# Performance work log

Measured on AMD Instinct MI355X. Metric: run time of the kernel, lower is better.

The kernel has to match this reference:

```python
import jax, jax.numpy as jnp
import numpy as np

B, H, W = 64, 224, 224
EPS = 1e-5


def setup_inputs() -> dict:
    key = jax.random.key(0)
    ks = jax.random.split(key, 8)
    n = lambda k, s, std: jax.random.normal(k, s, jnp.float32) * std
    return {
        "x": jax.random.normal(ks[0], (B, 1, H, W), jnp.float32),
        "conv1_w": n(ks[1], (24, 1, 3, 3), 0.2),
        "conv1_b": jnp.zeros((24,), jnp.float32),
        "bn1_g": jnp.ones((24,), jnp.float32),
        "bn1_b": jnp.zeros((24,), jnp.float32),
        "conv2_w": n(ks[2], (48, 24, 3, 3), 0.07),
        "conv2_b": jnp.zeros((48,), jnp.float32),
        "bn2_g": jnp.ones((48,), jnp.float32),
        "bn2_b": jnp.zeros((48,), jnp.float32),
        "fconv_w": n(ks[3], (48, 48, 56, 56), 0.003),
        "fconv_b": jnp.zeros((48,), jnp.float32),
        "lin1_w": n(ks[4], (24, 48), 0.02),
        "lin1_b": jnp.zeros((24,), jnp.float32),
        "lin2_w": n(ks[5], (4, 24), 0.01),
        "lin2_b": jnp.array([0.0, 0.0, 1.0, 0.0], jnp.float32),  # torch init: identity transform bias
    }


def conv2d(x, w, b):
    y = jax.lax.conv_general_dilated(x, w, (1, 1), ((1, 1), (1, 1)),
                                     dimension_numbers=("NCHW", "OIHW", "NCHW"))
    return y + b[None, :, None, None]


def batchnorm(x, g, b):
    # train-mode BN: batch statistics over (N, H, W), biased variance
    m = x.mean((0, 2, 3), keepdims=True)
    v = x.var((0, 2, 3), keepdims=True)
    return (x - m) * jax.lax.rsqrt(v + EPS) * g[None, :, None, None] + b[None, :, None, None]


def maxpool2(x):
    b, c, h, w = x.shape
    return x.reshape(b, c, h // 2, 2, w // 2, 2).max(axis=(3, 5))


def affine_grid(theta, h, w):
    # theta: [B,2,3]; align_corners=False normalized coords (torch default)
    xs = (jnp.arange(w, dtype=jnp.float32) * 2 + 1) / w - 1.0
    ys = (jnp.arange(h, dtype=jnp.float32) * 2 + 1) / h - 1.0
    gx, gy = jnp.meshgrid(xs, ys)                      # [H,W] each
    base = jnp.stack([gx, gy, jnp.ones_like(gx)], -1)  # [H,W,3] (x, y, 1)
    return jnp.einsum("bij,hwj->bhwi", theta, base)    # [B,H,W,2] -> (x, y)


def grid_sample(img, grid):
    # bilinear, zeros padding, align_corners=False (torch defaults)
    b, c, h, w = img.shape
    ix = ((grid[..., 0] + 1.0) * w - 1.0) * 0.5        # [B,H,W]
    iy = ((grid[..., 1] + 1.0) * h - 1.0) * 0.5
    x0 = jnp.floor(ix); y0 = jnp.floor(iy)
    x1 = x0 + 1.0; y1 = y0 + 1.0
    wx1 = ix - x0; wx0 = 1.0 - wx1
    wy1 = iy - y0; wy0 = 1.0 - wy1
    bidx = jnp.arange(b)[:, None, None]

    def tap(xf, yf, wgt):
        valid = (xf >= 0) & (xf < w) & (yf >= 0) & (yf < h)
        xi = jnp.clip(xf, 0, w - 1).astype(jnp.int32)
        yi = jnp.clip(yf, 0, h - 1).astype(jnp.int32)
        vals = img[bidx, :, yi, xi]                    # [B,H,W,C]
        return vals * (wgt * valid)[..., None]

    out = (tap(x0, y0, wx0 * wy0) + tap(x1, y0, wx1 * wy0)
           + tap(x0, y1, wx0 * wy1) + tap(x1, y1, wx1 * wy1))
    return jnp.transpose(out, (0, 3, 1, 2))            # [B,C,H,W]


def reference(x, conv1_w, conv1_b, bn1_g, bn1_b, conv2_w, conv2_b, bn2_g, bn2_b,
              fconv_w, fconv_b, lin1_w, lin1_b, lin2_w, lin2_b):
    b, _, h, w = x.shape
    x1 = maxpool2(jax.nn.relu(batchnorm(conv2d(x, conv1_w, conv1_b), bn1_g, bn1_b)))
    x1 = maxpool2(jax.nn.relu(batchnorm(conv2d(x1, conv2_w, conv2_b), bn2_g, bn2_b)))
    # final_conv with kernel 56 over a 56x56 map == full contraction
    feat = jnp.einsum("bchw,ochw->bo", x1, fconv_w) + fconv_b      # [B,48]
    theta4 = jax.nn.relu(feat @ lin1_w.T + lin1_b) @ lin2_w.T + lin2_b  # [B,4]
    tx, ty, scale, angle = theta4[:, 0], theta4[:, 1], theta4[:, 2], theta4[:, 3]
    c, s = jnp.cos(angle), jnp.sin(angle)
    # (T @ R @ S)[:, :2] built directly, fully vectorized over batch
    row0 = jnp.stack([scale * c, -scale * s, tx], -1)
    row1 = jnp.stack([scale * s, scale * c, ty], -1)
    theta = jnp.stack([row0, row1], 1)                 # [B,2,3]
    grid = affine_grid(theta, h, w)
    out = grid_sample(x, grid)
    return out, tx, ty, scale, angle
```

## Files before the change

### kernel.cpp

```cpp
#include <hip/hip_runtime.h>
#include <hip/hip_bf16.h>

#define NB 64
#define H0 224
#define W0 224
#define C1 24
#define C2 48
#define H1 112
#define W1 112
#define H2 56
#define W2 56
#define EPSV 1e-5f

#define WS_STATS1   0
#define WS_STATS2   432
#define WS_FEAT     1296
#define WS_B2       4368
#define WS_X2       11280
#define WS_X1       9645072
#define WS_NEED_BIG ((size_t)(WS_X1 + 9633792) * 4)
#define OUT0_ELEMS  (NB*H0*W0)

typedef _Float16 v8h __attribute__((ext_vector_type(8)));
typedef float    v4f __attribute__((ext_vector_type(4)));

static __device__ __forceinline__ unsigned short f2h(float v) {
    _Float16 h = (_Float16)v;
    unsigned short us;
    __builtin_memcpy(&us, &h, 2);
    return us;
}

__global__ __launch_bounds__(256) void k_init(const float* __restrict__ w2, float* __restrict__ ws)
{
    int t = blockIdx.x * 256 + threadIdx.x;
    if (t < WS_B2) ws[t] = 0.f;
    if (t < 13824) {
        int e = t & 7;
        int l = (t >> 3) & 63;
        int g = t >> 9;
        int q = l >> 4, ml = l & 15;
        int kp = g / 3, nt = g % 3;
        int ic = q * 8 + e;
        int oc = nt * 16 + ml;
        float v = (ic < C1) ? w2[(oc * C1 + ic) * 9 + kp] : 0.f;
        ((_Float16*)(ws + WS_B2))[t] = (_Float16)v;
    }
}

__global__ __launch_bounds__(256) void k_conv1_pool_stats4(
    const float* __restrict__ x, const float* __restrict__ w1, const float* __restrict__ b1,
    float* __restrict__ ws, _Float16* __restrict__ x1g)
{
    __shared__ float xt[34][36];
    __shared__ unsigned int outt[256][13];
    __shared__ float sred[2 * C1];

    const int tid = threadIdx.x;
    const int b = blockIdx.z;
    const int py0 = blockIdx.y * 16, px0 = blockIdx.x * 16;
    const int iy0 = 2 * py0 - 1, ix0 = 2 * px0 - 1;
    const float* xb = x + b * (H0 * W0);

    for (int li = tid; li < 34 * 34; li += 256) {
        int ry = li / 34, rx = li % 34;
        int gy = iy0 + ry, gx = ix0 + rx;
        bool ok = (gy >= 0) & (gy < H0) & (gx >= 0) & (gx < W0);
        xt[ry][rx] = ok ? xb[gy * W0 + gx] : 0.f;
    }

    const int wid = tid >> 6;
    const int lane = tid & 63;
    const int c0 = wid * 6;

    const int c0s = __builtin_amdgcn_readfirstlane(c0);
    const float* __restrict__ wps = w1 + c0s * 9;
    float wr[54], br[6];
#pragma unroll
    for (int k = 0; k < 54; k++) wr[k] = wps[k];
#pragma unroll
    for (int c = 0; c < 6; c++) br[c] = b1[c0s + c];

    __syncthreads();

    float s[6] = {0.f, 0.f, 0.f, 0.f, 0.f, 0.f};
    float q[6] = {0.f, 0.f, 0.f, 0.f, 0.f, 0.f};
    const int pc = lane & 15;
    const int pr0 = lane >> 4;

#pragma unroll
    for (int pp = 0; pp < 4; pp++) {
        const int pr = pr0 + 4 * pp;
        float patch[16];
#pragma unroll
        for (int i2 = 0; i2 < 4; i2++)
#pragma unroll
            for (int j2 = 0; j2 < 4; j2++)
                patch[i2 * 4 + j2] = xt[2 * pr + i2][2 * pc + j2];

        unsigned int pk[3];
#pragma unroll
        for (int cp = 0; cp < 3; cp++) {
            unsigned int pv = 0;
#pragma unroll
            for (int h = 0; h < 2; h++) {
                int c = 2 * cp + h;
                float m4 = -1e30f;
#pragma unroll
                for (int sy = 0; sy < 2; sy++)
#pragma unroll
                    for (int sx = 0; sx < 2; sx++) {
                        float a = br[c];
#pragma unroll
                        for (int ky = 0; ky < 3; ky++)
#pragma unroll
                            for (int kx = 0; kx < 3; kx++)
                                a = fmaf(patch[(sy + ky) * 4 + (sx + kx)], wr[c * 9 + ky * 3 + kx], a);
                        s[c] += a;
                        q[c] = fmaf(a, a, q[c]);
                        m4 = fmaxf(m4, a);
                    }
                pv |= ((unsigned int)f2h(m4)) << (16 * h);
            }
            pk[cp] = pv;
        }
        int pos = pr * 16 + pc;
        outt[pos][wid * 3 + 0] = pk[0];
        outt[pos][wid * 3 + 1] = pk[1];
        outt[pos][wid * 3 + 2] = pk[2];
    }

#pragma unroll
    for (int c = 0; c < 6; c++) {
#pragma unroll
        for (int off = 32; off > 0; off >>= 1) {
            s[c] += __shfl_down(s[c], off, 64);
            q[c] += __shfl_down(q[c], off, 64);
        }
    }
    if (lane == 0) {
#pragma unroll
        for (int c = 0; c < 6; c++) {
            sred[c0 + c] = s[c];
            sred[C1 + c0 + c] = q[c];
        }
    }
    __syncthreads();

    if (tid < 2 * C1) {
        int cp = (blockIdx.x + 7 * blockIdx.y + 49 * blockIdx.z) & 7;
        atomicAdd(&ws[WS_STATS1 + cp * 2 * C1 + tid], sred[tid]);
    }

    for (int u = tid; u < 768; u += 256) {
        int pos = u / 3, prt = u % 3;
        int pr = pos >> 4, pcc = pos & 15;
        long p = (long)(b * H1 + (py0 + pr)) * W1 + (px0 + pcc);
        uint4 v;
        v.x = outt[pos][4 * prt + 0];
        v.y = outt[pos][4 * prt + 1];
        v.z = outt[pos][4 * prt + 2];
        v.w = outt[pos][4 * prt + 3];
        *(uint4*)(x1g + p * C1 + prt * 8) = v;
    }
}

__global__ __launch_bounds__(256, 2) void k_conv2_fused3(
    const _Float16* __restrict__ x1g, const _Float16* __restrict__ bpp,
    const float* __restrict__ g1, const float* __restrict__ bb1,
    const float* __restrict__ b2,
    float* __restrict__ ws, float* __restrict__ pool)
{
    __shared__ __align__(16) _Float16 x1t[2][10][18][32];
    __shared__ float alds[C1], bflds[C1];
    __shared__ float sred[2 * C2];

    const int tid = threadIdx.x;
    const int w = tid >> 6;
    const int lane = tid & 63;
    const int ml = lane & 15;
    const int qq = lane >> 4;

    v8h B[9][3];
#pragma unroll
    for (int kp = 0; kp < 9; kp++)
#pragma unroll
        for (int nt = 0; nt < 3; nt++)
            B[kp][nt] = *(const v8h*)&bpp[((kp * 3 + nt) * 64 + lane) * 8];

    if (tid < C1) {
        float s = 0.f, q = 0.f;
#pragma unroll
        for (int i = 0; i < 8; i++) {
            s += ws[WS_STATS1 + i * 2 * C1 + tid];
            q += ws[WS_STATS1 + i * 2 * C1 + C1 + tid];
        }
        const float N = (float)(NB * H0 * W0);
        float m = s / N;
        float v = q / N - m * m;
        float a = g1[tid] / sqrtf(v + EPSV);
        alds[tid] = a;
        bflds[tid] = bb1[tid] - m * a;
    }
    if (tid < 2 * C2) sred[tid] = 0.f;

    float bias[3] = {b2[ml], b2[16 + ml], b2[32 + ml]};

    int spart[3], spr[3], spc[3]; bool swrite[3];
#pragma unroll
    for (int it3 = 0; it3 < 3; it3++) {
        int li = tid + it3 * 256;
        swrite[it3] = li < 720;
        spart[it3] = li & 3;
        int pos = li >> 2;
        spr[it3] = pos / 18;
        spc[it3] = pos % 18;
    }

    const int nb = gridDim.x;
    const int NTILE = 6272;
    int qn = NTILE / nb, rn = NTILE % nb;
    int start = (blockIdx.x < rn) ? blockIdx.x * (qn + 1)
                                  : rn * (qn + 1) + (blockIdx.x - rn) * qn;
    int cnt = (blockIdx.x < rn) ? qn + 1 : qn;

    float svacc[3] = {0.f, 0.f, 0.f}, qvacc[3] = {0.f, 0.f, 0.f};

    v8h raw[3];
    bool inb_n[3];
    {
        int t = start;
        int tb = t / 98, rem = t % 98;
        int ty = (rem / 7) * 8, txx = (rem % 7) * 16;
#pragma unroll
        for (int it3 = 0; it3 < 3; it3++) {
#pragma unroll
            for (int e = 0; e < 8; e++) raw[it3][e] = (_Float16)0.f;
            int gy = ty - 1 + spr[it3], gx = txx - 1 + spc[it3];
            inb_n[it3] = swrite[it3] & (spart[it3] < 3) &
                         (gy >= 0) & (gy < H1) & (gx >= 0) & (gx < W1);
            if (inb_n[it3])
                raw[it3] = *(const v8h*)&x1g[((tb * H1 + gy) * W1 + gx) * C1 + spart[it3] * 8];
        }
    }
    __syncthreads();

#pragma unroll
    for (int it3 = 0; it3 < 3; it3++) {
        if (swrite[it3]) {
            v8h r8;
            if (inb_n[it3]) {
#pragma unroll
                for (int e = 0; e < 8; e++) {
                    int c = spart[it3] * 8 + e;
                    float vv = fmaxf(fmaf((float)raw[it3][e], alds[c], bflds[c]), 0.f);
                    r8[e] = (_Float16)vv;
                }
            } else {
#pragma unroll
                for (int e = 0; e < 8; e++) r8[e] = (_Float16)0.f;
            }
            *(v8h*)&x1t[0][spr[it3]][spc[it3]][spart[it3] * 8] = r8;
        }
    }
    __syncthreads();

    for (int it = 0; it < cnt; it++) {
        const int cur = it & 1;
        const int t = start + it;
        const int tb = t / 98, rem = t % 98;
        const int ty = (rem / 7) * 8, txx = (rem % 7) * 16;

        const bool haveNext = (it + 1 < cnt);
        if (haveNext) {
            int t2 = t + 1;
            int nb2 = t2 / 98, rem2 = t2 % 98;
            int ny = (rem2 / 7) * 8, nx = (rem2 % 7) * 16;
#pragma unroll
            for (int it3 = 0; it3 < 3; it3++) {
#pragma unroll
                for (int e = 0; e < 8; e++) raw[it3][e] = (_Float16)0.f;
                int gy = ny - 1 + spr[it3], gx = nx - 1 + spc[it3];
                inb_n[it3] = swrite[it3] & (spart[it3] < 3) &
                             (gy >= 0) & (gy < H1) & (gx >= 0) & (gx < W1);
                if (inb_n[it3])
                    raw[it3] = *(const v8h*)&x1g[((nb2 * H1 + gy) * W1 + gx) * C1 + spart[it3] * 8];
            }
        }

        v4f acc[2][3];
#pragma unroll
        for (int mt = 0; mt < 2; mt++)
#pragma unroll
            for (int nt = 0; nt < 3; nt++)
                acc[mt][nt] = (v4f){0.f, 0.f, 0.f, 0.f};

#pragma unroll
        for (int kp = 0; kp < 9; kp++) {
            const int ky = kp / 3, kx = kp % 3;
#pragma unroll
            for (int mt = 0; mt < 2; mt++) {
                const int r = 2 * w + mt;
                v8h a = *(const v8h*)&x1t[cur][r + ky][ml + kx][qq * 8];
                acc[mt][0] = __builtin_amdgcn_mfma_f32_16x16x32_f16(a, B[kp][0], acc[mt][0], 0, 0, 0);
                acc[mt][1] = __builtin_amdgcn_mfma_f32_16x16x32_f16(a, B[kp][1], acc[mt][1], 0, 0, 0);
                acc[mt][2] = __builtin_amdgcn_mfma_f32_16x16x32_f16(a, B[kp][2], acc[mt][2], 0, 0, 0);
            }
        }

#pragma unroll
        for (int nt = 0; nt < 3; nt++) {
            int oc = nt * 16 + ml;
            float z[2][4];
#pragma unroll
            for (int mt = 0; mt < 2; mt++)
#pragma unroll
                for (int rg = 0; rg < 4; rg++) {
                    float val = acc[mt][nt][rg] + bias[nt];
                    z[mt][rg] = val;
                    svacc[nt] += val;
                    qvacc[nt] = fmaf(val, val, qvacc[nt]);
                }
            int py = (ty >> 1) + w;
#pragma unroll
            for (int j = 0; j < 2; j++) {
                float m = fmaxf(fmaxf(z[0][2 * j], z[0][2 * j + 1]),
                                fmaxf(z[1][2 * j], z[1][2 * j + 1]));
                int px = (txx >> 1) + qq * 2 + j;
                pool[((tb * C2 + oc) * H2 + py) * W2 + px] = m;
            }
        }

        if (haveNext) {
#pragma unroll
            for (int it3 = 0; it3 < 3; it3++) {
                if (swrite[it3]) {
                    v8h r8;
                    if (inb_n[it3]) {
#pragma unroll
                        for (int e = 0; e < 8; e++) {
                            int c = spart[it3] * 8 + e;
                            float vv = fmaxf(fmaf((float)raw[it3][e], alds[c], bflds[c]), 0.f);
                            r8[e] = (_Float16)vv;
                        }
                    } else {
#pragma unroll
                        for (int e = 0; e < 8; e++) r8[e] = (_Float16)0.f;
                    }
                    *(v8h*)&x1t[cur ^ 1][spr[it3]][spc[it3]][spart[it3] * 8] = r8;
                }
            }
        }
        __syncthreads();
    }

#pragma unroll
    for (int nt = 0; nt < 3; nt++) {
        float sv = svacc[nt], qv = qvacc[nt];
        sv += __shfl_xor(sv, 16, 64); qv += __shfl_xor(qv, 16, 64);
        sv += __shfl_xor(sv, 32, 64); qv += __shfl_xor(qv, 32, 64);
        if (qq == 0) {
            atomicAdd(&sred[nt * 16 + ml], sv);
            atomicAdd(&sred[C2 + nt * 16 + ml], qv);
        }
    }
    __syncthreads();
    if (tid < 2 * C2) {
        atomicAdd(&ws[WS_STATS2 + (blockIdx.x & 7) * 2 * C2 + tid], sred[tid]);
    }
}

#define FKC 128
__global__ __launch_bounds__(256) void k_fconv2(
    const float* __restrict__ pool, const float* __restrict__ ws,
    const float* __restrict__ g2, const float* __restrict__ bb2,
    const float* __restrict__ fw, float* __restrict__ part)
{
    __shared__ __align__(16) float fwt[C2][FKC + 4];
    __shared__ __align__(16) float x2t[NB][FKC + 4];
    __shared__ float csh[2 * C2];
    const int tid = threadIdx.x;
    if (tid < C2) {
        int c = tid;
        float s = 0.f, q = 0.f;
#pragma unroll
        for (int i = 0; i < 8; i++) {
            s += ws[WS_STATS2 + i * 2 * C2 + c];
            q += ws[WS_STATS2 + i * 2 * C2 + C2 + c];
        }
        const float N = (float)(NB * H1 * W1);
        float m = s / N;
        float v = q / N - m * m;
        float a = g2[c] / sqrtf(v + EPSV);
        csh[c] = a;
        csh[C2 + c] = bb2[c] - m * a;
    }
    const int k0 = blockIdx.x * FKC;

    for (int li = tid; li < C2 * (FKC / 4); li += 256) {
        int o = li / (FKC / 4), k4 = li % (FKC / 4);
        v4f v = *(const v4f*)&fw[o * 150528 + k0 + 4 * k4];
        *(v4f*)&fwt[o][4 * k4] = v;
    }
    __syncthreads();

    for (int li = tid; li < NB * (FKC / 4); li += 256) {
        int b = li / (FKC / 4), k4 = li % (FKC / 4);
        int kk = k0 + 4 * k4;
        v4f v = *(const v4f*)&pool[b * 150528 + kk];
        v4f r;
#pragma unroll
        for (int e = 0; e < 4; e++) {
            int c = (kk + e) / (H2 * W2);
            r[e] = fmaxf(fmaf(v[e], csh[c], csh[C2 + c]), 0.f);
        }
        *(v4f*)&x2t[b][4 * k4] = r;
    }
    __syncthreads();

    const int i = tid / 16, j = tid % 16;
    float acc[3][4] = {{0.f}};
    for (int k4 = 0; k4 < FKC / 4; k4++) {
        v4f fa[3], xv[4];
#pragma unroll
        for (int c = 0; c < 3; c++) fa[c] = *(const v4f*)&fwt[i + 16 * c][4 * k4];
#pragma unroll
        for (int d = 0; d < 4; d++) xv[d] = *(const v4f*)&x2t[j + 16 * d][4 * k4];
#pragma unroll
        for (int c = 0; c < 3; c++)
#pragma unroll
            for (int d = 0; d < 4; d++)
#pragma unroll
                for (int e = 0; e < 4; e++)
                    acc[c][d] = fmaf(fa[c][e], xv[d][e], acc[c][d]);
    }
    float* po = part + (long)blockIdx.x * (NB * C2);
#pragma unroll
    for (int c = 0; c < 3; c++)
#pragma unroll
        for (int d = 0; d < 4; d++)
            po[(j + 16 * d) * C2 + (i + 16 * c)] = acc[c][d];
}

__global__ __launch_bounds__(256) void k_freduce(const float* __restrict__ part, float* __restrict__ feat)
{
    const int t = (blockIdx.x % 12) * 256 + threadIdx.x;
    const int seg = blockIdx.x / 12;
    float s = 0.f;
    for (int bl = seg * 147; bl < (seg + 1) * 147; bl++)
        s += part[(long)bl * (NB * C2) + t];
    atomicAdd(&feat[t], s);
}

__global__ __launch_bounds__(256) void k_conv1_stats(
    const float* __restrict__ x, const float* __restrict__ w1, const float* __restrict__ b1,
    float* __restrict__ ws)
{
    float s[C1], q[C1];
#pragma unroll
    for (int c = 0; c < C1; c++) { s[c] = 0.f; q[c] = 0.f; }
    const int NT = gridDim.x * 256;
    const int total = NB * H0 * W0;
    for (int p = blockIdx.x * 256 + threadIdx.x; p < total; p += NT) {
        int b = p / (H0 * W0);
        int r = p % (H0 * W0);
        int y = r / W0;
        int xx = r % W0;
        const float* xb = x + b * (H0 * W0);
        float patch[9];
#pragma unroll
        for (int dy = 0; dy < 3; dy++)
#pragma unroll
            for (int dx = 0; dx < 3; dx++) {
                int yy = y + dy - 1, xc = xx + dx - 1;
                bool ok = (yy >= 0) & (yy < H0) & (xc >= 0) & (xc < W0);
                patch[dy * 3 + dx] = ok ? xb[yy * W0 + xc] : 0.f;
            }
#pragma unroll
        for (int c = 0; c < C1; c++) {
            const float* wp = w1 + c * 9;
            float a = b1[c];
#pragma unroll
            for (int k = 0; k < 9; k++) a = fmaf(patch[k], wp[k], a);
            s[c] += a;
            q[c] = fmaf(a, a, q[c]);
        }
    }
#pragma unroll
    for (int c = 0; c < C1; c++) {
#pragma unroll
        for (int off = 32; off > 0; off >>= 1) {
            s[c] += __shfl_down(s[c], off, 64);
            q[c] += __shfl_down(q[c], off, 64);
        }
    }
    __shared__ float sred[2 * C1];
    if (threadIdx.x < 2 * C1) sred[threadIdx.x] = 0.f;
    __syncthreads();
    if ((threadIdx.x & 63) == 0) {
#pragma unroll
        for (int c = 0; c < C1; c++) {
            atomicAdd(&sred[c], s[c]);
            atomicAdd(&sred[C1 + c], q[c]);
        }
    }
    __syncthreads();
    if (threadIdx.x < 2 * C1) {
        atomicAdd(&ws[WS_STATS1 + (blockIdx.x & 7) * 2 * C1 + threadIdx.x], sred[threadIdx.x]);
    }
}

__global__ __launch_bounds__(256, 2) void k_conv2_fused(
    const float* __restrict__ x, const float* __restrict__ w1, const float* __restrict__ b1,
    const float* __restrict__ g1, const float* __restrict__ bb1,
    const _Float16* __restrict__ bpp, const float* __restrict__ b2,
    float* __restrict__ ws, float* __restrict__ pool)
{
    __shared__ float xt[22][38];
    __shared__ __align__(16) _Float16 x1t[10][18][32];
    __shared__ __align__(16) _Float16 Blds[13824];
    __shared__ float wlds[C1 * 9];
    __shared__ float blds[C1], alds[C1], bflds[C1];
    __shared__ float sred[2 * C2];

    const int tid = threadIdx.x;
    const int b = blockIdx.z;
    const int y0 = blockIdx.y * 8;
    const int x0 = blockIdx.x * 16;
    const float* xb = x + b * (H0 * W0);

    for (int li = tid; li < 13824 / 8; li += 256)
        ((uint4*)Blds)[li] = ((const uint4*)bpp)[li];

    if (tid < C1 * 9) wlds[tid] = w1[tid];
    if (tid < C1) {
        float s = 0.f, q = 0.f;
#pragma unroll
        for (int i = 0; i < 8; i++) {
            s += ws[WS_STATS1 + i * 2 * C1 + tid];
            q += ws[WS_STATS1 + i * 2 * C1 + C1 + tid];
        }
        const float N = (float)(NB * H0 * W0);
        float m = s / N;
        float v = q / N - m * m;
        float a = g1[tid] / sqrtf(v + EPSV);
        blds[tid] = b1[tid];
        alds[tid] = a;
        bflds[tid] = bb1[tid] - m * a;
    }
    if (tid < 2 * C2) sred[tid] = 0.f;

    const int oy0 = 2 * y0 - 3, ox0 = 2 * x0 - 3;
    for (int li = tid; li < 22 * 38; li += 256) {
        int ry = li / 38, rx = li % 38;
        int gy = oy0 + ry, gx = ox0 + rx;
        bool ok = (gy >= 0) & (gy < H0) & (gx >= 0) & (gx < W0);
        xt[ry][rx] = ok ? xb[gy * W0 + gx] : 0.f;
    }
    __syncthreads();

    if (tid < 180) {
        int pr = tid / 18, pc = tid % 18;
        int gy = y0 - 1 + pr, gx = x0 - 1 + pc;
        bool valid = (gy >= 0) & (gy < H1) & (gx >= 0) & (gx < W1);
        float patch[16];
#pragma unroll
        for (int dy = 0; dy < 4; dy++)
#pragma unroll
            for (int dx = 0; dx < 4; dx++)
                patch[dy * 4 + dx] = xt[2 * pr + dy][2 * pc + dx];
        unsigned int* dst = (unsigned int*)&x1t[pr][pc][0];
#pragma unroll
        for (int cp = 0; cp < 12; cp++) {
            unsigned int pk = 0;
#pragma unroll
            for (int h = 0; h < 2; h++) {
                int c = 2 * cp + h;
                float m4 = -1e30f;
#pragma unroll
                for (int py = 0; py < 2; py++)
#pragma unroll
                    for (int px = 0; px < 2; px++) {
                        float a = blds[c];
#pragma unroll
                        for (int ky = 0; ky < 3; ky++)
#pragma unroll
                            for (int kx = 0; kx < 3; kx++)
                                a = fmaf(patch[(py + ky) * 4 + (px + kx)], wlds[c * 9 + ky * 3 + kx], a);
                        m4 = fmaxf(m4, fmaf(a, alds[c], bflds[c]));
                    }
                float v = valid ? fmaxf(m4, 0.f) : 0.f;
                pk |= ((unsigned int)f2h(v)) << (16 * h);
            }
            dst[cp] = pk;
        }
        dst[12] = 0; dst[13] = 0; dst[14] = 0; dst[15] = 0;
    }
    __syncthreads();

    const int w = tid >> 6;
    const int lane = tid & 63;
    const int ml = lane & 15;
    const int q = lane >> 4;

    v4f acc[2][3];
#pragma unroll
    for (int mt = 0; mt < 2; mt++)
#pragma unroll
        for (int nt = 0; nt < 3; nt++)
            acc[mt][nt] = (v4f){0.f, 0.f, 0.f, 0.f};

#pragma unroll
    for (int kp = 0; kp < 9; kp++) {
        const int ky = kp / 3, kx = kp % 3;
        v8h B0 = *(const v8h*)&Blds[((kp * 3 + 0) * 64 + lane) * 8];
        v8h B1 = *(const v8h*)&Blds[((kp * 3 + 1) * 64 + lane) * 8];
        v8h B2 = *(const v8h*)&Blds[((kp * 3 + 2) * 64 + lane) * 8];
#pragma unroll
        for (int mt = 0; mt < 2; mt++) {
            const int r = 2 * w + mt;
            v8h a = *(const v8h*)&x1t[r + ky][ml + kx][q * 8];
            acc[mt][0] = __builtin_amdgcn_mfma_f32_16x16x32_f16(a, B0, acc[mt][0], 0, 0, 0);
            acc[mt][1] = __builtin_amdgcn_mfma_f32_16x16x32_f16(a, B1, acc[mt][1], 0, 0, 0);
            acc[mt][2] = __builtin_amdgcn_mfma_f32_16x16x32_f16(a, B2, acc[mt][2], 0, 0, 0);
        }
    }

#pragma unroll
    for (int nt = 0; nt < 3; nt++) {
        int oc = nt * 16 + ml;
        float bias = b2[oc];
        float z[2][4];
        float sv = 0.f, qv = 0.f;
#pragma unroll
        for (int mt = 0; mt < 2; mt++)
#pragma unroll
            for (int rg = 0; rg < 4; rg++) {
                float val = acc[mt][nt][rg] + bias;
                z[mt][rg] = val;
                sv += val;
                qv = fmaf(val, val, qv);
            }
        sv += __shfl_xor(sv, 16, 64); qv += __shfl_xor(qv, 16, 64);
        sv += __shfl_xor(sv, 32, 64); qv += __shfl_xor(qv, 32, 64);
        if (q == 0) { atomicAdd(&sred[oc], sv); atomicAdd(&sred[C2 + oc], qv); }

        int py = (y0 >> 1) + w;
#pragma unroll
        for (int j = 0; j < 2; j++) {
            float m = fmaxf(fmaxf(z[0][2 * j], z[0][2 * j + 1]),
                            fmaxf(z[1][2 * j], z[1][2 * j + 1]));
            int px = (x0 >> 1) + q * 2 + j;
            pool[((b * C2 + oc) * H2 + py) * W2 + px] = m;
        }
    }
    __syncthreads();
    if (tid < 2 * C2) {
        int cp = (blockIdx.x + 7 * blockIdx.y + 31 * blockIdx.z) & 7;
        atomicAdd(&ws[WS_STATS2 + cp * 2 * C2 + tid], sred[tid]);
    }
}

#define KC 512
#define KSUB 128
__global__ __launch_bounds__(256) void k_fconv(
    const float* __restrict__ pool, const float* __restrict__ ws,
    const float* __restrict__ g2, const float* __restrict__ bb2,
    const float* __restrict__ fw, float* __restrict__ feat)
{
    __shared__ float fwt[C2][KSUB + 1];
    __shared__ float x2t[NB][KSUB + 1];
    __shared__ float csh[2 * C2];
    if (threadIdx.x < C2) {
        int c = threadIdx.x;
        float s = 0.f, q = 0.f;
#pragma unroll
        for (int i = 0; i < 8; i++) {
            s += ws[WS_STATS2 + i * 2 * C2 + c];
            q += ws[WS_STATS2 + i * 2 * C2 + C2 + c];
        }
        const float N = (float)(NB * H1 * W1);
        float m = s / N;
        float v = q / N - m * m;
        float a = g2[c] / sqrtf(v + EPSV);
        csh[c] = a;
        csh[C2 + c] = bb2[c] - m * a;
    }
    int k0 = blockIdx.x * KC;
    int i = threadIdx.x / 16, j = threadIdx.x % 16;
    float acc[3][4] = {{0.f}};
    for (int sub = 0; sub < KC / KSUB; sub++) {
        int kb = k0 + sub * KSUB;
        __syncthreads();
        for (int li = threadIdx.x; li < C2 * KSUB; li += 256) {
            int o = li / KSUB, k = li % KSUB;
            fwt[o][k] = fw[o * 150528 + kb + k];
        }
        for (int li = threadIdx.x; li < NB * KSUB; li += 256) {
            int b = li / KSUB, k = li % KSUB;
            int kk = kb + k;
            int c = kk / (H2 * W2);
            float v = pool[b * 150528 + kk];
            x2t[b][k] = fmaxf(fmaf(v, csh[c], csh[C2 + c]), 0.f);
        }
        __syncthreads();
        for (int k = 0; k < KSUB; k++) {
            float fa[3], xv[4];
#pragma unroll
            for (int c = 0; c < 3; c++) fa[c] = fwt[i + 16 * c][k];
#pragma unroll
            for (int d = 0; d < 4; d++) xv[d] = x2t[j + 16 * d][k];
#pragma unroll
            for (int c = 0; c < 3; c++)
#pragma unroll
                for (int d = 0; d < 4; d++)
                    acc[c][d] = fmaf(fa[c], xv[d], acc[c][d]);
        }
    }
#pragma unroll
    for (int c = 0; c < 3; c++)
#pragma unroll
        for (int d = 0; d < 4; d++)
            atomicAdd(&feat[(j + 16 * d) * C2 + (i + 16 * c)], acc[c][d]);
}

__global__ __launch_bounds__(256) void k_sample(
    const float* __restrict__ x, const float* __restrict__ feat, const float* __restrict__ fcb,
    const float* __restrict__ l1w, const float* __restrict__ l1b,
    const float* __restrict__ l2w, const float* __restrict__ l2b,
    float* __restrict__ out)
{
    __shared__ float hsh[24];
    __shared__ float th[4];
    int b = blockIdx.y;
    int tid = threadIdx.x;
    if (tid < 24) {
        float a = l1b[tid];
        for (int o = 0; o < C2; o++)
            a = fmaf(feat[b * C2 + o] + fcb[o], l1w[tid * C2 + o], a);
        hsh[tid] = fmaxf(a, 0.f);
    }
    __syncthreads();
    if (tid < 4) {
        float a = l2b[tid];
        for (int jj = 0; jj < 24; jj++) a = fmaf(hsh[jj], l2w[tid * 24 + jj], a);
        th[tid] = a;
        if (blockIdx.x == 0) out[OUT0_ELEMS + tid * NB + b] = a;
    }
    __syncthreads();

    int idx = blockIdx.x * 256 + tid;
    int i = idx / W0, j = idx % W0;
    float tx = th[0], ty = th[1], sc = th[2], an = th[3];
    float cc = cosf(an), ss = sinf(an);
    float t00 = sc * cc, t01 = -sc * ss, t10 = sc * ss, t11 = sc * cc;
    float xs = (2.f * (float)j + 1.f) / (float)W0 - 1.f;
    float ys = (2.f * (float)i + 1.f) / (float)H0 - 1.f;
    float gx = t00 * xs + t01 * ys + tx;
    float gy = t10 * xs + t11 * ys + ty;
    float ix = ((gx + 1.f) * (float)W0 - 1.f) * 0.5f;
    float iy = ((gy + 1.f) * (float)H0 - 1.f) * 0.5f;
    float x0 = floorf(ix), y0 = floorf(iy);
    float x1f = x0 + 1.f, y1f = y0 + 1.f;
    float wx1 = ix - x0, wx0 = 1.f - wx1;
    float wy1 = iy - y0, wy0 = 1.f - wy1;
    const float* xb = x + b * (H0 * W0);
    auto tap = [&](float xf, float yf, float wgt) -> float {
        bool valid = (xf >= 0.f) & (xf < (float)W0) & (yf >= 0.f) & (yf < (float)H0);
        int xi = (int)fminf(fmaxf(xf, 0.f), (float)(W0 - 1));
        int yi = (int)fminf(fmaxf(yf, 0.f), (float)(H0 - 1));
        return valid ? xb[yi * W0 + xi] * wgt : 0.f;
    };
    float o = tap(x0, y0, wx0 * wy0) + tap(x1f, y0, wx1 * wy0)
            + tap(x0, y1f, wx0 * wy1) + tap(x1f, y1f, wx1 * wy1);
    out[(b * H0 + i) * W0 + j] = o;
}

extern "C" void kernel_launch(void* const* d_in, const int* in_sizes, int n_in,
                              void* d_out, int out_size, void* d_ws, size_t ws_size,
                              hipStream_t stream)
{
    const float* x    = (const float*)d_in[0];
    const float* c1w  = (const float*)d_in[1];
    const float* c1b  = (const float*)d_in[2];
    const float* bn1g = (const float*)d_in[3];
    const float* bn1b = (const float*)d_in[4];
    const float* c2w  = (const float*)d_in[5];
    const float* c2b  = (const float*)d_in[6];
    const float* bn2g = (const float*)d_in[7];
    const float* bn2b = (const float*)d_in[8];
    const float* fw   = (const float*)d_in[9];
    const float* fcb  = (const float*)d_in[10];
    const float* l1w  = (const float*)d_in[11];
    const float* l1b  = (const float*)d_in[12];
    const float* l2w  = (const float*)d_in[13];
    const float* l2b  = (const float*)d_in[14];
    float* ws  = (float*)d_ws;
    float* out = (float*)d_out;

    k_init<<<dim3(54), 256, 0, stream>>>(c2w, ws);

    if (ws_size >= WS_NEED_BIG) {
        k_conv1_pool_stats4<<<dim3(7, 7, 64), 256, 0, stream>>>(
            x, c1w, c1b, ws, (_Float16*)(ws + WS_X1));
        k_conv2_fused3<<<dim3(512), 256, 0, stream>>>(
            (const _Float16*)(ws + WS_X1), (const _Float16*)(ws + WS_B2),
            bn1g, bn1b, c2b, ws, ws + WS_X2);
        k_fconv2<<<dim3(150528 / FKC), 256, 0, stream>>>(
            ws + WS_X2, ws, bn2g, bn2b, fw, ws + WS_X1);
        k_freduce<<<dim3(96), 256, 0, stream>>>(ws + WS_X1, ws + WS_FEAT);
    } else {
        k_conv1_stats<<<dim3(1024), 256, 0, stream>>>(x, c1w, c1b, ws);
        k_conv2_fused<<<dim3(7, 14, 64), 256, 0, stream>>>(
            x, c1w, c1b, bn1g, bn1b, (const _Float16*)(ws + WS_B2), c2b, ws, ws + WS_X2);
        k_fconv<<<dim3(150528 / KC), 256, 0, stream>>>(ws + WS_X2, ws, bn2g, bn2b, fw, ws + WS_FEAT);
    }
    k_sample<<<dim3(196, 64), 256, 0, stream>>>(x, ws + WS_FEAT, fcb, l1w, l1b, l2w, l2b, out);
}
```

Before: 260.0 us.

## Hoist theta MLP into its own kernel and halve the fconv K-chunk

Moves the small MLP that produces tx, ty, scale and angle out of the sampling kernel into a single-block k_theta kernel, so it runs once per call instead of redundantly in every sampling block. k_sample2 then only reads the four precomputed values per batch. The full-contraction fconv K-chunk drops from 128 to 64 with its inner loop fully unrolled, which doubles the block count, and the partial-sum reduction grid doubles to match. The cost is an extra kernel launch and more partial buffers to reduce.

Measured after the change: 281.0 us. 1.08x slower.

```diff
diff --git a/kernel.cpp b/kernel.cpp
--- a/kernel.cpp
+++ b/kernel.cpp
@@ -370,8 +370,8 @@
     }
 }
 
-#define FKC 128
-__global__ __launch_bounds__(256) void k_fconv2(
+#define FKC 64
+__global__ __launch_bounds__(256) void k_fconv3(
     const float* __restrict__ pool, const float* __restrict__ ws,
     const float* __restrict__ g2, const float* __restrict__ bb2,
     const float* __restrict__ fw, float* __restrict__ part)
@@ -420,6 +420,7 @@
 
     const int i = tid / 16, j = tid % 16;
     float acc[3][4] = {{0.f}};
+#pragma unroll
     for (int k4 = 0; k4 < FKC / 4; k4++) {
         v4f fa[3], xv[4];
 #pragma unroll
@@ -442,7 +443,7 @@
             po[(j + 16 * d) * C2 + (i + 16 * c)] = acc[c][d];
 }
 
-__global__ __launch_bounds__(256) void k_freduce(const float* __restrict__ part, float* __restrict__ feat)
+__global__ __launch_bounds__(256) void k_freduce2(const float* __restrict__ part, float* __restrict__ feat)
 {
     const int t = (blockIdx.x % 12) * 256 + threadIdx.x;
     const int seg = blockIdx.x / 12;
@@ -450,6 +451,67 @@
     for (int bl = seg * 147; bl < (seg + 1) * 147; bl++)
         s += part[(long)bl * (NB * C2) + t];
     atomicAdd(&feat[t], s);
+}
+
+__global__ __launch_bounds__(64) void k_theta(
+    const float* __restrict__ feat, const float* __restrict__ fcb,
+    const float* __restrict__ l1w, const float* __restrict__ l1b,
+    const float* __restrict__ l2w, const float* __restrict__ l2b,
+    float* __restrict__ th4, float* __restrict__ out)
+{
+    const int b = threadIdx.x;
+    float f[C2];
+#pragma unroll
+    for (int o = 0; o < C2; o++) f[o] = feat[b * C2 + o] + fcb[o];
+    float h[24];
+#pragma unroll
+    for (int jj = 0; jj < 24; jj++) {
+        float a = l1b[jj];
+#pragma unroll
+        for (int o = 0; o < C2; o++) a = fmaf(f[o], l1w[jj * C2 + o], a);
+        h[jj] = fmaxf(a, 0.f);
+    }
+#pragma unroll
+    for (int k = 0; k < 4; k++) {
+        float a = l2b[k];
+#pragma unroll
+        for (int jj = 0; jj < 24; jj++) a = fmaf(h[jj], l2w[k * 24 + jj], a);
+        th4[k * NB + b] = a;
+        out[OUT0_ELEMS + k * NB + b] = a;
+    }
+}
+
+__global__ __launch_bounds__(256) void k_sample2(
+    const float* __restrict__ x, const float* __restrict__ th4, float* __restrict__ out)
+{
+    const int b = blockIdx.y;
+    const float tx = th4[0 * NB + b], ty = th4[1 * NB + b];
+    const float sc = th4[2 * NB + b], an = th4[3 * NB + b];
+
+    int idx = blockIdx.x * 256 + threadIdx.x;
+    int i = idx / W0, j = idx % W0;
+    float cc = cosf(an), ss = sinf(an);
+    float t00 = sc * cc, t01 = -sc * ss, t10 = sc * ss, t11 = sc * cc;
+    float xs = (2.f * (float)j + 1.f) / (float)W0 - 1.f;
+    float ys = (2.f * (float)i + 1.f) / (float)H0 - 1.f;
+    float gx = t00 * xs + t01 * ys + tx;
+    float gy = t10 * xs + t11 * ys + ty;
+    float ix = ((gx + 1.f) * (float)W0 - 1.f) * 0.5f;
+    float iy = ((gy + 1.f) * (float)H0 - 1.f) * 0.5f;
+    float x0 = floorf(ix), y0 = floorf(iy);
+    float x1f = x0 + 1.f, y1f = y0 + 1.f;
+    float wx1 = ix - x0, wx0 = 1.f - wx1;
+    float wy1 = iy - y0, wy0 = 1.f - wy1;
+    const float* xb = x + b * (H0 * W0);
+    auto tap = [&](float xf, float yf, float wgt) -> float {
+        bool valid = (xf >= 0.f) & (xf < (float)W0) & (yf >= 0.f) & (yf < (float)H0);
+        int xi = (int)fminf(fmaxf(xf, 0.f), (float)(W0 - 1));
+        int yi = (int)fminf(fmaxf(yf, 0.f), (float)(H0 - 1));
+        return valid ? xb[yi * W0 + xi] * wgt : 0.f;
+    };
+    float o = tap(x0, y0, wx0 * wy0) + tap(x1f, y0, wx1 * wy0)
+            + tap(x0, y1f, wx0 * wy1) + tap(x1f, y1f, wx1 * wy1);
+    out[(b * H0 + i) * W0 + j] = o;
 }
 
 __global__ __launch_bounds__(256) void k_conv1_stats(
@@ -806,14 +868,17 @@
         k_conv2_fused3<<<dim3(512), 256, 0, stream>>>(
             (const _Float16*)(ws + WS_X1), (const _Float16*)(ws + WS_B2),
             bn1g, bn1b, c2b, ws, ws + WS_X2);
-        k_fconv2<<<dim3(150528 / FKC), 256, 0, stream>>>(
+        k_fconv3<<<dim3(150528 / FKC), 256, 0, stream>>>(
             ws + WS_X2, ws, bn2g, bn2b, fw, ws + WS_X1);
-        k_freduce<<<dim3(96), 256, 0, stream>>>(ws + WS_X1, ws + WS_FEAT);
+        k_freduce2<<<dim3(192), 256, 0, stream>>>(ws + WS_X1, ws + WS_FEAT);
+        k_theta<<<dim3(1), 64, 0, stream>>>(
+            ws + WS_FEAT, fcb, l1w, l1b, l2w, l2b, ws + WS_B2, out);
+        k_sample2<<<dim3(196, 64), 256, 0, stream>>>(x, ws + WS_B2, out);
     } else {
         k_conv1_stats<<<dim3(1024), 256, 0, stream>>>(x, c1w, c1b, ws);
         k_conv2_fused<<<dim3(7, 14, 64), 256, 0, stream>>>(
             x, c1w, c1b, bn1g, bn1b, (const _Float16*)(ws + WS_B2), c2b, ws, ws + WS_X2);
         k_fconv<<<dim3(150528 / KC), 256, 0, stream>>>(ws + WS_X2, ws, bn2g, bn2b, fw, ws + WS_FEAT);
-    }
-    k_sample<<<dim3(196, 64), 256, 0, stream>>>(x, ws + WS_FEAT, fcb, l1w, l1b, l2w, l2b, out);
-}
+        k_sample<<<dim3(196, 64), 256, 0, stream>>>(x, ws + WS_FEAT, fcb, l1w, l1b, l2w, l2b, out);
+    }
+}
```
